# Optimization experiments

Hardware: AMD Instinct MI355X
Metric: run time of the kernel (lower is better)

Reference implementation:

```python
import jax, jax.numpy as jnp
import numpy as np

HIDDEN = 2048
N_HEADS = 16
N_KV = 2
HEAD_DIM = 256
ROT_DIM = 64  # partial_rotary_factor 0.25
EPS = 1e-6
B, S = 2, 2048


def _rms_norm(x, w, eps=EPS):
    var = jnp.mean(jnp.square(x), axis=-1, keepdims=True)
    return x * jax.lax.rsqrt(var + eps) * w


def _rotate_half(x):
    x1, x2 = jnp.split(x, 2, axis=-1)
    return jnp.concatenate([-x2, x1], axis=-1)


def setup_inputs() -> dict:
    key = jax.random.key(0)
    ks = jax.random.split(key, 8)
    hidden_states = jax.random.normal(ks[0], (B, S, HIDDEN), dtype=jnp.float32)
    # real RoPE cos/sin over rotary_dim (HF convention: freqs duplicated)
    inv_freq = 1.0 / (10000.0 ** (np.arange(0, ROT_DIM, 2, dtype=np.float32) / ROT_DIM))
    pos = np.arange(S, dtype=np.float32)
    ang = np.einsum('s,f->sf', pos, inv_freq)                # [S, ROT_DIM/2]
    emb = np.concatenate([ang, ang], axis=-1)                # [S, ROT_DIM]
    cos = jnp.asarray(np.broadcast_to(np.cos(emb), (B, S, ROT_DIM)))
    sin = jnp.asarray(np.broadcast_to(np.sin(emb), (B, S, ROT_DIM)))
    sc = 0.02
    Wq = jax.random.normal(ks[1], (N_HEADS * HEAD_DIM * 2, HIDDEN), dtype=jnp.float32) * sc
    Wk = jax.random.normal(ks[2], (N_KV * HEAD_DIM, HIDDEN), dtype=jnp.float32) * sc
    Wv = jax.random.normal(ks[3], (N_KV * HEAD_DIM, HIDDEN), dtype=jnp.float32) * sc
    Wo = jax.random.normal(ks[4], (HIDDEN, N_HEADS * HEAD_DIM), dtype=jnp.float32) * sc
    q_norm_w = jnp.ones((HEAD_DIM,), dtype=jnp.float32)
    k_norm_w = jnp.ones((HEAD_DIM,), dtype=jnp.float32)
    return {"hidden_states": hidden_states, "cos": cos, "sin": sin,
            "Wq": Wq, "Wk": Wk, "Wv": Wv, "Wo": Wo,
            "q_norm_w": q_norm_w, "k_norm_w": k_norm_w}


def reference(hidden_states, cos, sin, Wq, Wk, Wv, Wo, q_norm_w, k_norm_w):
    b, s, _ = hidden_states.shape
    # gated Q projection: [b, s, n_heads, 2*head_dim] -> query, gate
    qg = jnp.einsum('bsd,od->bso', hidden_states, Wq).reshape(b, s, N_HEADS, 2 * HEAD_DIM)
    q, gate = jnp.split(qg, 2, axis=-1)                      # each [b,s,H,D]
    gate = gate.reshape(b, s, N_HEADS * HEAD_DIM)
    k = jnp.einsum('bsd,od->bso', hidden_states, Wk).reshape(b, s, N_KV, HEAD_DIM)
    v = jnp.einsum('bsd,od->bso', hidden_states, Wv).reshape(b, s, N_KV, HEAD_DIM)
    # per-head RMSNorm before RoPE
    q = _rms_norm(q, q_norm_w)
    k = _rms_norm(k, k_norm_w)
    # partial RoPE on first ROT_DIM dims
    c = cos[:, :, None, :]
    sn = sin[:, :, None, :]
    q_rot, q_pass = q[..., :ROT_DIM], q[..., ROT_DIM:]
    k_rot, k_pass = k[..., :ROT_DIM], k[..., ROT_DIM:]
    q_rot = q_rot * c + _rotate_half(q_rot) * sn
    k_rot = k_rot * c + _rotate_half(k_rot) * sn
    q = jnp.concatenate([q_rot, q_pass], axis=-1)
    k = jnp.concatenate([k_rot, k_pass], axis=-1)
    # GQA: repeat kv heads
    rep = N_HEADS // N_KV
    k = jnp.repeat(k, rep, axis=2)
    v = jnp.repeat(v, rep, axis=2)
    scale = 1.0 / jnp.sqrt(jnp.float32(HEAD_DIM))
    scores = jnp.einsum('bqhd,bkhd->bhqk', q, k) * scale
    causal = jnp.tril(jnp.ones((s, s), dtype=bool))
    scores = jnp.where(causal[None, None], scores, jnp.finfo(scores.dtype).min)
    probs = jax.nn.softmax(scores, axis=-1)
    attn = jnp.einsum('bhqk,bkhd->bqhd', probs, v).reshape(b, s, N_HEADS * HEAD_DIM)
    attn = attn * jax.nn.sigmoid(gate)
    return jnp.einsum('bsi,oi->bso', attn, Wo)
```

## Files before the change

### kernel.cpp

```cpp
#include <hip/hip_runtime.h>
#include <stdint.h>

typedef unsigned short u16;
typedef __bf16 bf16x8 __attribute__((ext_vector_type(8)));
typedef float f32x4 __attribute__((ext_vector_type(4)));
typedef u16 u16x4 __attribute__((ext_vector_type(4)));
typedef u16 u16x8 __attribute__((ext_vector_type(8)));

__device__ __forceinline__ u16 f2b(float f) {
    unsigned u = __builtin_bit_cast(unsigned, f);
    u = u + 0x7FFFu + ((u >> 16) & 1u);
    return (u16)(u >> 16);
}
__device__ __forceinline__ float b2f(u16 b) {
    return __builtin_bit_cast(float, (unsigned)b << 16);
}

__device__ __forceinline__ void glds16(const u16* g, u16* l) {
    __builtin_amdgcn_global_load_lds(
        (const __attribute__((address_space(1))) void*)g,
        (__attribute__((address_space(3))) void*)l,
        16, 0, 0);
}

template <int N> __device__ __forceinline__ void waitvm() {
    if constexpr (N == 0)      asm volatile("s_waitcnt vmcnt(0)" ::: "memory");
    else if constexpr (N == 2) asm volatile("s_waitcnt vmcnt(2)" ::: "memory");
    else if constexpr (N == 3) asm volatile("s_waitcnt vmcnt(3)" ::: "memory");
    else if constexpr (N == 4) asm volatile("s_waitcnt vmcnt(4)" ::: "memory");
    else if constexpr (N == 6) asm volatile("s_waitcnt vmcnt(6)" ::: "memory");
    else if constexpr (N == 8) asm volatile("s_waitcnt vmcnt(8)" ::: "memory");
}

__global__ __launch_bounds__(256) void cast_bf16(const float* __restrict__ src,
                                                 u16* __restrict__ dst, int n) {
    int i = (blockIdx.x * 256 + threadIdx.x) * 4;
    if (i >= n) return;
    f32x4 v = *(const f32x4*)(src + i);
    u16x4 o;
    o.x = f2b(v.x); o.y = f2b(v.y); o.z = f2b(v.z); o.w = f2b(v.w);
    *(u16x4*)(dst + i) = o;
}

template <int OUT_BF16>
__global__ __launch_bounds__(256) void gemm_bt(const u16* __restrict__ A,
                                               const u16* __restrict__ Bt,
                                               void* __restrict__ Cout,
                                               int M, int N, int K) {
    __shared__ u16 As[128 * 32];
    __shared__ u16 Bs[128 * 32];
    const int tid  = threadIdx.x;
    const int w    = tid >> 6;
    const int lane = tid & 63;
    const int quad = lane >> 4;
    const int ml   = lane & 15;
    const long bm  = (long)blockIdx.y * 128;
    const long bn  = (long)blockIdx.x * 128;
    const int wm   = (w >> 1) * 64;
    const int wn   = (w & 1) * 64;
    const int grow = lane >> 2;
    const int gcol = (lane & 3) * 8;

    const u16* Ag = A  + (bm + w * 16 + grow) * (long)K + gcol;
    const u16* Bg = Bt + (bn + w * 16 + grow) * (long)K + gcol;
    u16* lAs0 = &As[(w * 16) * 32];
    u16* lAs1 = &As[(64 + w * 16) * 32];
    u16* lBs0 = &Bs[(w * 16) * 32];
    u16* lBs1 = &Bs[(64 + w * 16) * 32];

    const f32x4 fz = {0.f, 0.f, 0.f, 0.f};
    f32x4 acc[4][4];
#pragma unroll
    for (int i = 0; i < 4; ++i)
#pragma unroll
        for (int j = 0; j < 4; ++j) acc[i][j] = fz;

    for (int k0 = 0; k0 < K; k0 += 32) {
        __syncthreads();
        glds16(Ag + k0,                lAs0);
        glds16(Ag + 64 * (long)K + k0, lAs1);
        glds16(Bg + k0,                lBs0);
        glds16(Bg + 64 * (long)K + k0, lBs1);
        __builtin_amdgcn_s_waitcnt(0);
        __syncthreads();
        bf16x8 af[4], bfr[4];
#pragma unroll
        for (int mt = 0; mt < 4; ++mt)
            af[mt] = *(const bf16x8*)&As[(wm + mt * 16 + ml) * 32 + quad * 8];
#pragma unroll
        for (int nt = 0; nt < 4; ++nt)
            bfr[nt] = *(const bf16x8*)&Bs[(wn + nt * 16 + ml) * 32 + quad * 8];
#pragma unroll
        for (int mt = 0; mt < 4; ++mt)
#pragma unroll
            for (int nt = 0; nt < 4; ++nt)
                acc[mt][nt] = __builtin_amdgcn_mfma_f32_16x16x32_bf16(
                    af[mt], bfr[nt], acc[mt][nt], 0, 0, 0);
    }
#pragma unroll
    for (int mt = 0; mt < 4; ++mt)
#pragma unroll
        for (int nt = 0; nt < 4; ++nt)
#pragma unroll
            for (int r = 0; r < 4; ++r) {
                long row = bm + wm + mt * 16 + quad * 4 + r;
                long col = bn + wn + nt * 16 + ml;
                float v = acc[mt][nt][r];
                if (OUT_BF16) ((u16*)Cout)[row * N + col] = f2b(v);
                else          ((float*)Cout)[row * N + col] = v;
            }
}

template <int OUT_BF16, int BN>
__global__ __launch_bounds__(512, 4) void gemm_pipe(const u16* __restrict__ A,
                                                    const u16* __restrict__ Bt,
                                                    void* __restrict__ Cout,
                                                    int M, int N, int K, int nbx) {
    (void)M;
    constexpr int NF  = BN / 64;
    constexpr int ASZ = 128 * 32;
    constexpr int BSZ = BN * 32;
    constexpr int LPT = 1 + BN / 128;
    __shared__ u16 sm[3][ASZ + BSZ];

    const int tid  = threadIdx.x;
    const int w    = tid >> 6;
    const int lane = tid & 63;
    const int quad = lane >> 4;
    const int ml   = lane & 15;
    const int wm   = (w >> 2) * 64;
    const int wn   = (w & 3) * (BN / 4);

    const int nwg = gridDim.x;
    const int q8 = nwg >> 3, r8 = nwg & 7;
    const int xcd = blockIdx.x & 7, loc = blockIdx.x >> 3;
    const int wg  = (xcd < r8 ? xcd * (q8 + 1) : r8 * (q8 + 1) + (xcd - r8) * q8) + loc;
    const int per = nbx * 8;
    const int gid = wg / per, win = wg % per;
    const long bm = (long)(gid * 8 + (win & 7)) * 128;
    const long bn = (long)(win >> 3) * BN;

    const int  srow = w * 16 + (lane >> 2);
    const int  scc  = (lane & 3) ^ ((lane >> 3) & 3);
    const u16* Ag0  = A  + (bm + srow) * (long)K + scc * 8;
    const u16* Bg0  = Bt + (bn + srow) * (long)K + scc * 8;
    const u16* Bg1  = (BN == 256) ? Bg0 + 128 * (long)K : Bg0;
    const int  ldsw = w * 512;

    const int ccr  = quad ^ ((ml >> 1) & 3);
    const int aoff = (wm + ml) * 32 + ccr * 8;
    const int boff = (wn + ml) * 32 + ccr * 8;

    const f32x4 fz = {0.f, 0.f, 0.f, 0.f};
    f32x4 acc[4][NF];
#pragma unroll
    for (int i = 0; i < 4; ++i)
#pragma unroll
        for (int j = 0; j < NF; ++j) acc[i][j] = fz;

    const int NT = K >> 5;

#define STAGE(tt)                                                      \
    {                                                                  \
        u16* base = &sm[(tt) % 3][0];                                  \
        const long ko = (long)(tt) * 32;                               \
        glds16(Ag0 + ko, base + ldsw);                                 \
        glds16(Bg0 + ko, base + ASZ + ldsw);                           \
        if (BN == 256) glds16(Bg1 + ko, base + ASZ + 4096 + ldsw);     \
    }

    STAGE(0); STAGE(1);

    for (int t = 0; t < NT; ++t) {
        if (t + 1 < NT) waitvm<LPT>();
        else            waitvm<0>();
        __builtin_amdgcn_s_barrier();
        __builtin_amdgcn_sched_barrier(0);
        if (t + 2 < NT) STAGE(t + 2);

        const u16* Ab = &sm[t % 3][0];
        const u16* Bb = Ab + ASZ;
        bf16x8 af[4], bfr[NF];
#pragma unroll
        for (int mt = 0; mt < 4; ++mt)
            af[mt] = *(const bf16x8*)(Ab + aoff + mt * 512);
#pragma unroll
        for (int nt = 0; nt < NF; ++nt)
            bfr[nt] = *(const bf16x8*)(Bb + boff + nt * 512);

        __builtin_amdgcn_s_setprio(1);
#pragma unroll
        for (int mt = 0; mt < 4; ++mt)
#pragma unroll
            for (int nt = 0; nt < NF; ++nt)
                acc[mt][nt] = __builtin_amdgcn_mfma_f32_16x16x32_bf16(
                    af[mt], bfr[nt], acc[mt][nt], 0, 0, 0);
        __builtin_amdgcn_s_setprio(0);
    }
#undef STAGE

#pragma unroll
    for (int mt = 0; mt < 4; ++mt)
#pragma unroll
        for (int nt = 0; nt < NF; ++nt)
#pragma unroll
            for (int r = 0; r < 4; ++r) {
                long row = bm + wm + mt * 16 + quad * 4 + r;
                long col = bn + wn + nt * 16 + ml;
                float v = acc[mt][nt][r];
                if (OUT_BF16) ((u16*)Cout)[row * N + col] = f2b(v);
                else          ((float*)Cout)[row * N + col] = v;
            }
}

__global__ __launch_bounds__(64) void norm_rope(const u16* __restrict__ qgk,
                                                const float* __restrict__ cosp,
                                                const float* __restrict__ sinp,
                                                const float* __restrict__ qw,
                                                const float* __restrict__ kw,
                                                u16* __restrict__ qf,
                                                u16* __restrict__ kf) {
    const int t = blockIdx.x;
    const int u = blockIdx.y;
    const int lane = threadIdx.x;
    const int b = t >> 11, s = t & 2047;
    const u16* src; const float* wgt; u16* dst;
    if (u < 16) {
        src = qgk + (long)t * 8704 + u * 512;
        wgt = qw;
        dst = qf + ((long)(b * 16 + u) * 2048 + s) * 256;
    } else {
        int kh = u - 16;
        src = qgk + (long)t * 8704 + 8192 + kh * 256;
        wgt = kw;
        dst = kf + ((long)(b * 2 + kh) * 2048 + s) * 256;
    }
    const int d0 = lane * 4;
    u16x4 raw = *(const u16x4*)(src + d0);
    float x0 = b2f(raw.x), x1 = b2f(raw.y), x2 = b2f(raw.z), x3 = b2f(raw.w);
    float ss = x0 * x0 + x1 * x1 + x2 * x2 + x3 * x3;
    for (int off = 32; off; off >>= 1) ss += __shfl_xor(ss, off, 64);
    float inv = rsqrtf(ss * (1.0f / 256.0f) + 1e-6f);
    float n0 = x0 * inv * wgt[d0 + 0];
    float n1 = x1 * inv * wgt[d0 + 1];
    float n2 = x2 * inv * wgt[d0 + 2];
    float n3 = x3 * inv * wgt[d0 + 3];
    float p0 = __shfl_xor(n0, 8, 64);
    float p1 = __shfl_xor(n1, 8, 64);
    float p2 = __shfl_xor(n2, 8, 64);
    float p3 = __shfl_xor(n3, 8, 64);
    if (lane < 16) {
        f32x4 c  = *(const f32x4*)(cosp + (long)t * 64 + d0);
        f32x4 sn = *(const f32x4*)(sinp + (long)t * 64 + d0);
        float sgn = (lane < 8) ? -1.f : 1.f;
        n0 = n0 * c[0] + sgn * p0 * sn[0];
        n1 = n1 * c[1] + sgn * p1 * sn[1];
        n2 = n2 * c[2] + sgn * p2 * sn[2];
        n3 = n3 * c[3] + sgn * p3 * sn[3];
    }
    const float qs = (u < 16) ? 0.0625f : 1.0f;
    n0 *= qs; n1 *= qs; n2 *= qs; n3 *= qs;
    u16x4 o;
    o.x = f2b(n0); o.y = f2b(n1); o.z = f2b(n2); o.w = f2b(n3);
    *(u16x4*)(dst + d0) = o;
}

__global__ __launch_bounds__(256) void attn_fused(const u16* __restrict__ qf,
                                                  const u16* __restrict__ kf,
                                                  const u16* __restrict__ vt,
                                                  const u16* __restrict__ qgk,
                                                  u16* __restrict__ attn_g) {
    __shared__ u16 Ks[64 * 256];
    __shared__ u16 Vt[256 * 64];
    __shared__ u16 P[64 * 64];
    const int flat = blockIdx.x;
    const int qt = 31 - (flat >> 5);
    const int h  = flat & 15;
    const int b  = (flat >> 4) & 1;
    const int kh = h >> 3;
    const int tid = threadIdx.x;
    const int w = tid >> 6, lane = tid & 63;
    const int quad = lane >> 4, ml = lane & 15;
    const int qrow = qt * 64 + w * 16;

    const u16* qptr = qf + ((long)(b * 16 + h) * 2048 + qrow + ml) * 256;
    bf16x8 qfrag[8];
#pragma unroll
    for (int dd = 0; dd < 8; ++dd)
        qfrag[dd] = *(const bf16x8*)(qptr + dd * 32 + quad * 8);

    const f32x4 fz = {0.f, 0.f, 0.f, 0.f};
    f32x4 oacc[16];
#pragma unroll
    for (int i = 0; i < 16; ++i) oacc[i] = fz;
    float lsum[4] = {0.f, 0.f, 0.f, 0.f};

    const u16* kbp = kf + (long)(b * 2 + kh) * 2048 * 256;
    const u16* vbp = vt + (long)kh * 256 * 4096 + (long)b * 2048;

    const int krow = tid >> 5;
    const int kswz = (tid & 31) ^ krow;
    const int vrow = tid >> 3;
    const int vswz = (tid & 7) ^ (vrow & 7);
    u16* ldsKw = &Ks[w * 512];
    u16* ldsVw = &Vt[w * 512];

    const int m7 = ml & 7;

    const int nkt = qt + 1;
    for (int kt = 0; kt < nkt; ++kt) {
        const int kb = kt * 64;
        __syncthreads();
#pragma unroll
        for (int i = 0; i < 8; ++i)
            glds16(kbp + (long)(kb + i * 8 + krow) * 256 + kswz * 8,
                   ldsKw + i * 2048);
#pragma unroll
        for (int i = 0; i < 8; ++i)
            glds16(vbp + (long)(i * 32 + vrow) * 4096 + kb + vswz * 8,
                   ldsVw + i * 2048);
        waitvm<8>();
        __builtin_amdgcn_s_barrier();
        __builtin_amdgcn_sched_barrier(0);

        f32x4 sacc[4];
#pragma unroll
        for (int i = 0; i < 4; ++i) sacc[i] = fz;
#pragma unroll
        for (int dd = 0; dd < 8; ++dd) {
            const int ck = (dd * 4 + quad) ^ m7;
            bf16x8 kf0 = *(const bf16x8*)&Ks[(0 * 16 + ml) * 256 + ck * 8];
            bf16x8 kf1 = *(const bf16x8*)&Ks[(1 * 16 + ml) * 256 + ck * 8];
            bf16x8 kf2 = *(const bf16x8*)&Ks[(2 * 16 + ml) * 256 + ck * 8];
            bf16x8 kf3 = *(const bf16x8*)&Ks[(3 * 16 + ml) * 256 + ck * 8];
            __builtin_amdgcn_s_setprio(1);
            sacc[0] = __builtin_amdgcn_mfma_f32_16x16x32_bf16(qfrag[dd], kf0, sacc[0], 0, 0, 0);
            sacc[1] = __builtin_amdgcn_mfma_f32_16x16x32_bf16(qfrag[dd], kf1, sacc[1], 0, 0, 0);
            sacc[2] = __builtin_amdgcn_mfma_f32_16x16x32_bf16(qfrag[dd], kf2, sacc[2], 0, 0, 0);
            sacc[3] = __builtin_amdgcn_mfma_f32_16x16x32_bf16(qfrag[dd], kf3, sacc[3], 0, 0, 0);
            __builtin_amdgcn_s_setprio(0);
        }

        const bool diag = (kt == qt);
#pragma unroll
        for (int nt = 0; nt < 4; ++nt)
#pragma unroll
            for (int r = 0; r < 4; ++r) {
                float sv = sacc[nt][r];
                const int row = w * 16 + quad * 4 + r;
                if (diag) {
                    int col = nt * 16 + ml;
                    sv = (col > (quad * 4 + r + w * 16)) ? -1e30f : sv;
                }
                float pv = __expf(sv - 16.0f);
                lsum[r] += pv;
                const int chk = (nt * 2 + (ml >> 3)) ^ ((quad * 4 + r) & 7);
                P[row * 64 + chk * 8 + m7] = f2b(pv);
            }

        waitvm<0>();
        __builtin_amdgcn_s_barrier();
        __builtin_amdgcn_sched_barrier(0);

#pragma unroll
        for (int ks = 0; ks < 2; ++ks) {
            const int ck = (ks * 4 + quad) ^ m7;
            bf16x8 pfrag = *(const bf16x8*)&P[(w * 16 + ml) * 64 + ck * 8];
            __builtin_amdgcn_s_setprio(1);
#pragma unroll
            for (int dt = 0; dt < 16; ++dt) {
                bf16x8 vfrag = *(const bf16x8*)&Vt[(dt * 16 + ml) * 64 + ck * 8];
                oacc[dt] = __builtin_amdgcn_mfma_f32_16x16x32_bf16(pfrag, vfrag, oacc[dt], 0, 0, 0);
            }
            __builtin_amdgcn_s_setprio(0);
        }
    }

#pragma unroll
    for (int off = 1; off < 16; off <<= 1)
#pragma unroll
        for (int r = 0; r < 4; ++r) lsum[r] += __shfl_xor(lsum[r], off, 64);

#pragma unroll
    for (int dt = 0; dt < 16; ++dt)
#pragma unroll
        for (int r = 0; r < 4; ++r) {
            int srow = qrow + quad * 4 + r;
            long tok = (long)b * 2048 + srow;
            int d = dt * 16 + ml;
            float o = oacc[dt][r] / lsum[r];
            float g = b2f(qgk[tok * 8704 + h * 512 + 256 + d]);
            float gv = o / (1.f + __expf(-g));
            attn_g[tok * 4096 + h * 256 + d] = f2b(gv);
        }
}

extern "C" void kernel_launch(void* const* d_in, const int* in_sizes, int n_in,
                              void* d_out, int out_size, void* d_ws, size_t ws_size,
                              hipStream_t stream) {
    (void)in_sizes; (void)n_in; (void)out_size;
    const float* hidden = (const float*)d_in[0];
    const float* cosp   = (const float*)d_in[1];
    const float* sinp   = (const float*)d_in[2];
    const float* Wq     = (const float*)d_in[3];
    const float* Wk     = (const float*)d_in[4];
    const float* Wv     = (const float*)d_in[5];
    const float* Wo     = (const float*)d_in[6];
    const float* qw     = (const float*)d_in[7];
    const float* kw     = (const float*)d_in[8];
    float* out = (float*)d_out;

    char* p = (char*)d_ws;
    u16* h_bf   = (u16*)p; p += (size_t)8388608 * 2;
    u16* Wqk_bf = (u16*)p; p += (size_t)17825792 * 2;
    u16* Wv_bf  = (u16*)p; p += (size_t)1048576 * 2;
    u16* Wo_bf  = (u16*)p; p += (size_t)8388608 * 2;
    u16* qgk    = (u16*)p; p += (size_t)35651584 * 2;
    u16* v_t    = (u16*)p; p += (size_t)2097152 * 2;
    u16* q_f    = (u16*)p; p += (size_t)16777216 * 2;
    u16* k_f    = (u16*)p; p += (size_t)2097152 * 2;
    u16* attn_g = (u16*)p; p += (size_t)16777216 * 2;
    if ((size_t)(p - (char*)d_ws) > ws_size) return;

    cast_bf16<<<8192,  256, 0, stream>>>(hidden, h_bf, 8388608);
    cast_bf16<<<16384, 256, 0, stream>>>(Wq, Wqk_bf, 16777216);
    cast_bf16<<<1024,  256, 0, stream>>>(Wk, Wqk_bf + (size_t)8192 * 2048, 1048576);
    cast_bf16<<<1024,  256, 0, stream>>>(Wv, Wv_bf, 1048576);
    cast_bf16<<<8192,  256, 0, stream>>>(Wo, Wo_bf, 8388608);

    gemm_pipe<1, 256><<<dim3(1088), 512, 0, stream>>>(h_bf, Wqk_bf, qgk, 4096, 8704, 2048, 34);
    gemm_bt<1><<<dim3(32, 4), 256, 0, stream>>>(Wv_bf, h_bf, v_t, 512, 4096, 2048);

    norm_rope<<<dim3(4096, 18), 64, 0, stream>>>(qgk, cosp, sinp, qw, kw, q_f, k_f);

    attn_fused<<<dim3(1024), 256, 0, stream>>>(q_f, k_f, v_t, qgk, attn_g);

    gemm_pipe<0, 128><<<dim3(512), 512, 0, stream>>>(attn_g, Wo_bf, out, 4096, 2048, 4096, 16);
}
```

Measured before the change: 605.1 us.

## Widen attention blocks to 128 query rows, merge casts, batch norm_rope waves

The attention kernel now runs 8 waves per block covering 128 query rows, so each K/V tile loaded into LDS serves twice as many queries. This halves total K/V global traffic, at the cost of coarser causal work granularity and fewer blocks. The five weight and activation casts are merged into one grid-stride kernel to cut launch overhead. norm_rope packs four tokens per 256-thread block instead of one token per 64-thread block.

```diff
diff --git a/kernel.cpp b/kernel.cpp
--- a/kernel.cpp
+++ b/kernel.cpp
@@ -32,14 +32,29 @@
     else if constexpr (N == 8) asm volatile("s_waitcnt vmcnt(8)" ::: "memory");
 }
 
-__global__ __launch_bounds__(256) void cast_bf16(const float* __restrict__ src,
-                                                 u16* __restrict__ dst, int n) {
-    int i = (blockIdx.x * 256 + threadIdx.x) * 4;
-    if (i >= n) return;
-    f32x4 v = *(const f32x4*)(src + i);
-    u16x4 o;
-    o.x = f2b(v.x); o.y = f2b(v.y); o.z = f2b(v.z); o.w = f2b(v.w);
-    *(u16x4*)(dst + i) = o;
+__global__ __launch_bounds__(256) void cast_all(const float* __restrict__ h,
+                                                const float* __restrict__ wq,
+                                                const float* __restrict__ wk,
+                                                const float* __restrict__ wv,
+                                                const float* __restrict__ wo,
+                                                u16* __restrict__ h_bf,
+                                                u16* __restrict__ wqk_bf,
+                                                u16* __restrict__ wv_bf,
+                                                u16* __restrict__ wo_bf) {
+    const long total  = 35651584;
+    const long stride = (long)gridDim.x * 256 * 4;
+    for (long i = ((long)blockIdx.x * 256 + threadIdx.x) * 4; i < total; i += stride) {
+        const float* s; u16* d; long off;
+        if (i < 8388608)        { s = h;  d = h_bf;             off = i; }
+        else if (i < 25165824)  { s = wq; d = wqk_bf;           off = i - 8388608; }
+        else if (i < 26214400)  { s = wk; d = wqk_bf + 16777216; off = i - 25165824; }
+        else if (i < 27262976)  { s = wv; d = wv_bf;            off = i - 26214400; }
+        else                    { s = wo; d = wo_bf;            off = i - 27262976; }
+        f32x4 v = *(const f32x4*)(s + off);
+        u16x4 o;
+        o.x = f2b(v.x); o.y = f2b(v.y); o.z = f2b(v.z); o.w = f2b(v.w);
+        *(u16x4*)(d + off) = o;
+    }
 }
 
 template <int OUT_BF16>
@@ -213,16 +228,16 @@
             }
 }
 
-__global__ __launch_bounds__(64) void norm_rope(const u16* __restrict__ qgk,
-                                                const float* __restrict__ cosp,
-                                                const float* __restrict__ sinp,
-                                                const float* __restrict__ qw,
-                                                const float* __restrict__ kw,
-                                                u16* __restrict__ qf,
-                                                u16* __restrict__ kf) {
-    const int t = blockIdx.x;
+__global__ __launch_bounds__(256) void norm_rope(const u16* __restrict__ qgk,
+                                                 const float* __restrict__ cosp,
+                                                 const float* __restrict__ sinp,
+                                                 const float* __restrict__ qw,
+                                                 const float* __restrict__ kw,
+                                                 u16* __restrict__ qf,
+                                                 u16* __restrict__ kf) {
+    const int t = blockIdx.x * 4 + (threadIdx.x >> 6);
     const int u = blockIdx.y;
-    const int lane = threadIdx.x;
+    const int lane = threadIdx.x & 63;
     const int b = t >> 11, s = t & 2047;
     const u16* src; const float* wgt; u16* dst;
     if (u < 16) {
@@ -265,23 +280,25 @@
     *(u16x4*)(dst + d0) = o;
 }
 
-__global__ __launch_bounds__(256) void attn_fused(const u16* __restrict__ qf,
-                                                  const u16* __restrict__ kf,
-                                                  const u16* __restrict__ vt,
-                                                  const u16* __restrict__ qgk,
-                                                  u16* __restrict__ attn_g) {
+__global__ __launch_bounds__(512, 4) void attn_fused(const u16* __restrict__ qf,
+                                                     const u16* __restrict__ kf,
+                                                     const u16* __restrict__ vt,
+                                                     const u16* __restrict__ qgk,
+                                                     u16* __restrict__ attn_g) {
     __shared__ u16 Ks[64 * 256];
     __shared__ u16 Vt[256 * 64];
-    __shared__ u16 P[64 * 64];
+    __shared__ u16 P[128 * 64];
     const int flat = blockIdx.x;
-    const int qt = 31 - (flat >> 5);
+    const int qt = 15 - (flat >> 5);
     const int h  = flat & 15;
     const int b  = (flat >> 4) & 1;
     const int kh = h >> 3;
     const int tid = threadIdx.x;
     const int w = tid >> 6, lane = tid & 63;
     const int quad = lane >> 4, ml = lane & 15;
-    const int qrow = qt * 64 + w * 16;
+    const int wh = w >> 2, wq = w & 3;
+    const int qrow = qt * 128 + wh * 64 + wq * 16;
+    const int dtile = 2 * qt + wh;
 
     const u16* qptr = qf + ((long)(b * 16 + h) * 2048 + qrow + ml) * 256;
     bf16x8 qfrag[8];
@@ -298,28 +315,28 @@
     const u16* kbp = kf + (long)(b * 2 + kh) * 2048 * 256;
     const u16* vbp = vt + (long)kh * 256 * 4096 + (long)b * 2048;
 
-    const int krow = tid >> 5;
-    const int kswz = (tid & 31) ^ krow;
-    const int vrow = tid >> 3;
-    const int vswz = (tid & 7) ^ (vrow & 7);
-    u16* ldsKw = &Ks[w * 512];
-    u16* ldsVw = &Vt[w * 512];
+    const int krow7 = (tid >> 5) & 7;
+    const int kswz  = (tid & 31) ^ krow7;
+    const int vrow7 = (tid >> 3) & 7;
+    const int vswz  = (tid & 7) ^ vrow7;
+    const int krow  = tid >> 5;
+    const int vrow  = tid >> 3;
 
     const int m7 = ml & 7;
 
-    const int nkt = qt + 1;
+    const int nkt = 2 * qt + 2;
     for (int kt = 0; kt < nkt; ++kt) {
         const int kb = kt * 64;
         __syncthreads();
 #pragma unroll
-        for (int i = 0; i < 8; ++i)
-            glds16(kbp + (long)(kb + i * 8 + krow) * 256 + kswz * 8,
-                   ldsKw + i * 2048);
-#pragma unroll
-        for (int i = 0; i < 8; ++i)
-            glds16(vbp + (long)(i * 32 + vrow) * 4096 + kb + vswz * 8,
-                   ldsVw + i * 2048);
-        waitvm<8>();
+        for (int i = 0; i < 4; ++i)
+            glds16(kbp + (long)(kb + i * 16 + krow) * 256 + kswz * 8,
+                   Ks + i * 4096 + w * 512);
+#pragma unroll
+        for (int i = 0; i < 4; ++i)
+            glds16(vbp + (long)(i * 64 + vrow) * 4096 + kb + vswz * 8,
+                   Vt + i * 4096 + w * 512);
+        waitvm<4>();
         __builtin_amdgcn_s_barrier();
         __builtin_amdgcn_sched_barrier(0);
 
@@ -341,21 +358,21 @@
             __builtin_amdgcn_s_setprio(0);
         }
 
-        const bool diag = (kt == qt);
+        const bool maskt = (kt >= dtile);
 #pragma unroll
         for (int nt = 0; nt < 4; ++nt)
 #pragma unroll
             for (int r = 0; r < 4; ++r) {
                 float sv = sacc[nt][r];
-                const int row = w * 16 + quad * 4 + r;
-                if (diag) {
-                    int col = nt * 16 + ml;
-                    sv = (col > (quad * 4 + r + w * 16)) ? -1e30f : sv;
+                if (maskt) {
+                    int rel = wq * 16 + quad * 4 + r + (dtile - kt) * 64;
+                    sv = (nt * 16 + ml > rel) ? -1e30f : sv;
                 }
                 float pv = __expf(sv - 16.0f);
                 lsum[r] += pv;
+                const int prow = w * 16 + quad * 4 + r;
                 const int chk = (nt * 2 + (ml >> 3)) ^ ((quad * 4 + r) & 7);
-                P[row * 64 + chk * 8 + m7] = f2b(pv);
+                P[prow * 64 + chk * 8 + m7] = f2b(pv);
             }
 
         waitvm<0>();
@@ -422,18 +439,15 @@
     u16* attn_g = (u16*)p; p += (size_t)16777216 * 2;
     if ((size_t)(p - (char*)d_ws) > ws_size) return;
 
-    cast_bf16<<<8192,  256, 0, stream>>>(hidden, h_bf, 8388608);
-    cast_bf16<<<16384, 256, 0, stream>>>(Wq, Wqk_bf, 16777216);
-    cast_bf16<<<1024,  256, 0, stream>>>(Wk, Wqk_bf + (size_t)8192 * 2048, 1048576);
-    cast_bf16<<<1024,  256, 0, stream>>>(Wv, Wv_bf, 1048576);
-    cast_bf16<<<8192,  256, 0, stream>>>(Wo, Wo_bf, 8388608);
+    cast_all<<<2048, 256, 0, stream>>>(hidden, Wq, Wk, Wv, Wo,
+                                       h_bf, Wqk_bf, Wv_bf, Wo_bf);
 
     gemm_pipe<1, 256><<<dim3(1088), 512, 0, stream>>>(h_bf, Wqk_bf, qgk, 4096, 8704, 2048, 34);
     gemm_bt<1><<<dim3(32, 4), 256, 0, stream>>>(Wv_bf, h_bf, v_t, 512, 4096, 2048);
 
-    norm_rope<<<dim3(4096, 18), 64, 0, stream>>>(qgk, cosp, sinp, qw, kw, q_f, k_f);
-
-    attn_fused<<<dim3(1024), 256, 0, stream>>>(q_f, k_f, v_t, qgk, attn_g);
+    norm_rope<<<dim3(1024, 18), 256, 0, stream>>>(qgk, cosp, sinp, qw, kw, q_f, k_f);
+
+    attn_fused<<<dim3(512), 512, 0, stream>>>(q_f, k_f, v_t, qgk, attn_g);
 
     gemm_pipe<0, 128><<<dim3(512), 512, 0, stream>>>(attn_g, Wo_bf, out, 4096, 2048, 4096, 16);
 }
```

After: 794.1 us. +31.2%, slower.
